# Kernel tuning notes

Hardware: AMD Instinct MI355X
Metric: run time of the kernel (lower is better)

## Reference

```python
import jax, jax.numpy as jnp
import numpy as np

NUM_EMBEDDINGS = 1024
EMBEDDING_DIM = 256
BETA = 0.25


def setup_inputs() -> dict:
    key = jax.random.key(0)
    k1, k2 = jax.random.split(key)
    inputs = jax.random.normal(k1, (32, EMBEDDING_DIM, 64, 64), dtype=jnp.float32)
    # codebook init: uniform(-1/K, 1/K), matching nn.Embedding init in the module
    embedding = jax.random.uniform(
        k2, (NUM_EMBEDDINGS, EMBEDDING_DIM), dtype=jnp.float32,
        minval=-1.0 / NUM_EMBEDDINGS, maxval=1.0 / NUM_EMBEDDINGS)
    return {"inputs": inputs, "embedding": embedding, "beta": BETA}


def reference(inputs, embedding, beta):
    # inputs: [B, D, H, W] -> [B, H, W, D]
    x = jnp.transpose(inputs, (0, 2, 3, 1))
    in_shape = x.shape
    flat = x.reshape(-1, embedding.shape[1])  # [N, D]
    dist = (jnp.sum(flat * flat, axis=1, keepdims=True)
            + jnp.sum(embedding * embedding, axis=1)
            - 2.0 * flat @ embedding.T)
    codebook_indices = jnp.argmin(dist, axis=1)  # [N]
    quantized = embedding[codebook_indices].reshape(in_shape)  # [B,H,W,D]
    sg = jax.lax.stop_gradient
    e_latent_loss = beta * jnp.mean((sg(quantized) - x) ** 2)
    q_latent_loss = jnp.mean((quantized - sg(x)) ** 2)
    loss = e_latent_loss + q_latent_loss
    # straight-through estimator
    quantized_st = x + sg(quantized - x)
    return loss, jnp.transpose(quantized_st, (0, 3, 1, 2))
```

## Files before the change

### kernel.cpp

```cpp
#include <hip/hip_runtime.h>


#define DIN 256

typedef __attribute__((ext_vector_type(8))) short short8;
typedef __attribute__((ext_vector_type(4))) float float4v;
typedef __attribute__((ext_vector_type(4))) unsigned short ushort4v;

static __device__ __forceinline__ unsigned short f2bf(float f) {
  unsigned int u = __float_as_uint(f);
  unsigned int r = (u + 0x7fffu + ((u >> 16) & 1u)) >> 16;
  return (unsigned short)r;
}

__global__ void vq_prep(const float* __restrict__ e,
                        unsigned short* __restrict__ e_pre,
                        float* __restrict__ norms) {
  int wave = threadIdx.x >> 6, lane = threadIdx.x & 63;
  int k = blockIdx.x * 4 + wave;
  const float4v* src = (const float4v*)(e + k * DIN);
  float4v v = src[lane];
  float ss = v[0]*v[0] + v[1]*v[1] + v[2]*v[2] + v[3]*v[3];
  ushort4v pk;
  pk[0] = f2bf(v[0]); pk[1] = f2bf(v[1]); pk[2] = f2bf(v[2]); pk[3] = f2bf(v[3]);
  int t = k >> 5, kL = k & 31;
  int cc = lane >> 1, half = lane & 1;
  int s = cc ^ (kL & 7);
  *(ushort4v*)(e_pre + t * 8192 + kL * 256 + s * 8 + half * 4) = pk;
  #pragma unroll
  for (int m = 1; m < 64; m <<= 1) ss += __shfl_xor(ss, m, 64);
  if (lane == 0) norms[k] = ss;
}

#define BARRIER_RAW() do { asm volatile("" ::: "memory"); \
  __builtin_amdgcn_s_barrier(); asm volatile("" ::: "memory"); } while (0)

__global__ void __launch_bounds__(512, 4)
vq_main(const float* __restrict__ xin, const float* __restrict__ e_fp,
        const unsigned short* __restrict__ e_pre,
        const float* __restrict__ norms,
        float* __restrict__ out, float* __restrict__ loss_acc) {
  __shared__ char smem[41024];
  unsigned short* xs = (unsigned short*)smem;
  float* qs  = (float*)smem;
  float* nrm = (float*)(smem + 32768);
  float* xnp = (float*)(smem + 36864);
  int*   fi  = (int*)(smem + 38912);
  float* xna = (float*)(smem + 39936);
  float* prt = (float*)(smem + 40960);

  const int tid  = threadIdx.x;
  const int wave = tid >> 6, lane = tid & 63;
  const int m16  = lane & 15, quad = lane >> 4;
  const int line0 = blockIdx.x * 4;

  nrm[tid] = norms[tid];
  nrm[tid + 512] = norms[tid + 512];

  short8 areg[16];
  const int wL  = wave >> 1;
  const int w32 = (wave & 1) * 32;
  {
    const int w  = tid & 63;
    const int cg = wave;
    for (int L = 0; L < 4; ++L) {
      int line = line0 + L;
      const float* xl = xin + (line >> 6) * 1048576 + (line & 63) * 64;
      __syncthreads();
      float ss = 0.0f;
      #pragma unroll
      for (int q8 = 0; q8 < 4; ++q8) {
        int cc = cg * 4 + q8;
        short8 pk;
        #pragma unroll
        for (int ii = 0; ii < 8; ++ii) {
          float xv = xl[(cc * 8 + ii) * 4096 + w];
          ss += xv * xv;
          pk[ii] = (short)f2bf(xv);
        }
        *(short8*)(xs + w * 256 + 8 * (cc ^ (w & 7))) = pk;
      }
      xnp[w * 8 + cg] = ss;
      __syncthreads();
      if (wL == L) {
        #pragma unroll
        for (int i = 0; i < 2; ++i)
          #pragma unroll
          for (int kk = 0; kk < 8; ++kk) {
            int r = w32 + i * 16 + m16;
            areg[i * 8 + kk] =
                *(short8*)(xs + r * 256 + 8 * ((kk * 4 + quad) ^ (r & 7)));
          }
      }
      if (tid < 64) {
        float s2 = 0.0f;
        #pragma unroll
        for (int u = 0; u < 8; ++u) s2 += xnp[tid * 8 + u];
        xna[L * 64 + tid] = s2;
      }
    }
  }
  __syncthreads();

  float bestv[2][4];
  int   besti[2][4];
  #pragma unroll
  for (int i = 0; i < 2; ++i)
    #pragma unroll
    for (int r = 0; r < 4; ++r) { bestv[i][r] = INFINITY; besti[i][r] = 0; }

  auto stage = [&](int t, int buf) {
    const char* src = (const char*)e_pre + t * 16384;
    char* dst = smem + buf * 16384;
    #pragma unroll
    for (int j = 0; j < 2; ++j) {
      int off = (j * 8 + wave) * 1024 + lane * 16;
      __builtin_amdgcn_global_load_lds(
          (const __attribute__((address_space(1))) unsigned int*)(src + off),
          (__attribute__((address_space(3))) unsigned int*)(dst + off),
          16, 0, 0);
    }
  };

  stage(0, 0);
  for (int t = 0; t < 32; ++t) {
    if (t < 31) {
      stage(t + 1, (t + 1) & 1);
      asm volatile("s_waitcnt vmcnt(2)" ::: "memory");
    } else {
      asm volatile("s_waitcnt vmcnt(0)" ::: "memory");
    }
    BARRIER_RAW();
    const unsigned short* eb = (const unsigned short*)(smem + (t & 1) * 16384);
    #pragma unroll
    for (int j = 0; j < 2; ++j) {
      int cL = j * 16 + m16;
      float4v a0 = (float4v)(0.0f), a1 = (float4v)(0.0f);
      #pragma unroll
      for (int kk = 0; kk < 8; ++kk) {
        short8 bfr = *(const short8*)(eb + cL * 256 + 8 * ((kk * 4 + quad) ^ (cL & 7)));
        a0 = __builtin_amdgcn_mfma_f32_16x16x32_bf16(areg[kk],     bfr, a0, 0, 0, 0);
        a1 = __builtin_amdgcn_mfma_f32_16x16x32_bf16(areg[8 + kk], bfr, a1, 0, 0, 0);
      }
      int col = t * 32 + cL;
      float nj = nrm[col];
      #pragma unroll
      for (int r = 0; r < 4; ++r) {
        float s0 = nj - 2.0f * a0[r];
        if (s0 < bestv[0][r]) { bestv[0][r] = s0; besti[0][r] = col; }
        float s1 = nj - 2.0f * a1[r];
        if (s1 < bestv[1][r]) { bestv[1][r] = s1; besti[1][r] = col; }
      }
    }
    BARRIER_RAW();
  }

  #pragma unroll
  for (int msk = 1; msk <= 8; msk <<= 1) {
    #pragma unroll
    for (int i = 0; i < 2; ++i)
      #pragma unroll
      for (int r = 0; r < 4; ++r) {
        float ov = __shfl_xor(bestv[i][r], msk, 64);
        int   oi = __shfl_xor(besti[i][r], msk, 64);
        if (ov < bestv[i][r] || (ov == bestv[i][r] && oi < besti[i][r])) {
          bestv[i][r] = ov; besti[i][r] = oi;
        }
      }
  }

  float lsum = 0.0f;
  if (m16 == 0) {
    #pragma unroll
    for (int i = 0; i < 2; ++i)
      #pragma unroll
      for (int r = 0; r < 4; ++r) {
        int row = wave * 32 + i * 16 + quad * 4 + r;
        fi[row] = besti[i][r];
        lsum += bestv[i][r] + xna[row];
      }
  }
  #pragma unroll
  for (int msk = 1; msk < 64; msk <<= 1) lsum += __shfl_xor(lsum, msk, 64);
  if (lane == 0) prt[wave] = lsum;
  __syncthreads();
  if (tid == 0) {
    float s = 0.0f;
    #pragma unroll
    for (int u = 0; u < 8; ++u) s += prt[u];
    atomicAdd(loss_acc, s);
  }

  for (int L = 0; L < 4; ++L) {
    int line = line0 + L;
    float* ob = out + 1 + (line >> 6) * 1048576 + (line & 63) * 64;
    int w = tid >> 3, dg = tid & 7;
    int idx = fi[L * 64 + w];
    const float* er = e_fp + idx * 256;
    int swz = (w >> 2) & 7;
    for (int h2 = 0; h2 < 2; ++h2) {
      #pragma unroll
      for (int j = 0; j < 4; ++j) {
        int c = dg + 8 * j;
        float4v qv = *(const float4v*)(er + h2 * 128 + c * 4);
        *(float4v*)(qs + w * 128 + (c ^ swz) * 4) = qv;
      }
      __syncthreads();
      #pragma unroll
      for (int it = 0; it < 4; ++it) {
        int dl = it * 32 + wave * 4 + quad;
        int slot = (dl >> 2) ^ (m16 & 7);
        float4v ov;
        #pragma unroll
        for (int k = 0; k < 4; ++k)
          ov[k] = qs[(m16 * 4 + k) * 128 + slot * 4 + (dl & 3)];
        *(float4v*)(ob + (h2 * 128 + dl) * 4096 + m16 * 4) = ov;
      }
      __syncthreads();
    }
  }
}

__global__ void vq_fin(const float* __restrict__ loss_acc,
                       const float* __restrict__ beta,
                       float* __restrict__ out) {
  out[0] = (1.0f + beta[0]) * loss_acc[0] / 33554432.0f;
}

extern "C" void kernel_launch(void* const* d_in, const int* in_sizes, int n_in,
                              void* d_out, int out_size, void* d_ws, size_t ws_size,
                              hipStream_t stream) {
  const float* xin  = (const float*)d_in[0];
  const float* emb  = (const float*)d_in[1];
  const float* beta = (const float*)d_in[2];
  float* out = (float*)d_out;
  float* loss_acc = (float*)d_ws;
  float* norms = (float*)((char*)d_ws + 4096);
  unsigned short* e_pre = (unsigned short*)((char*)d_ws + 8192);

  hipMemsetAsync(d_ws, 0, 4, stream);
  vq_prep<<<256, 256, 0, stream>>>(emb, e_pre, norms);
  vq_main<<<512, 512, 0, stream>>>(xin, emb, e_pre, norms, out, loss_acc);
  vq_fin<<<1, 1, 0, stream>>>(loss_acc, beta, out);
}
```

Measured before the change: 359.8 us.

## Halve block to 4 waves, each owning 64 rows loaded directly into registers

Moves the block from 8 waves to 4. Each wave now handles one full image line of 64 rows with four MFMA accumulator sets per codebook fragment, so every LDS-loaded codebook fragment feeds twice as many MFMAs. The input tile is read straight from global memory into A-fragment registers rather than staged through swizzled LDS, and the codebook prefetch now starts before that load. The output transpose is rewritten as a column-major LDS write followed by contiguous float4 stores. Costs are much higher register pressure (32 short8 A fragments plus 16 accumulators), 64KB of LDS per block, and lower occupancy.

```diff
diff --git a/kernel.cpp b/kernel.cpp
--- a/kernel.cpp
+++ b/kernel.cpp
@@ -35,98 +35,83 @@
 #define BARRIER_RAW() do { asm volatile("" ::: "memory"); \
   __builtin_amdgcn_s_barrier(); asm volatile("" ::: "memory"); } while (0)
 
-__global__ void __launch_bounds__(512, 4)
+__global__ void __launch_bounds__(256, 2)
 vq_main(const float* __restrict__ xin, const float* __restrict__ e_fp,
         const unsigned short* __restrict__ e_pre,
         const float* __restrict__ norms,
         float* __restrict__ out, float* __restrict__ loss_acc) {
-  __shared__ char smem[41024];
-  unsigned short* xs = (unsigned short*)smem;
+  __shared__ char smem[65536];
   float* qs  = (float*)smem;
   float* nrm = (float*)(smem + 32768);
-  float* xnp = (float*)(smem + 36864);
-  int*   fi  = (int*)(smem + 38912);
-  float* xna = (float*)(smem + 39936);
-  float* prt = (float*)(smem + 40960);
+  float* xna = (float*)(smem + 36864);
+  int*   fi  = (int*)(smem + 37888);
+  float* prt = (float*)(smem + 38912);
 
   const int tid  = threadIdx.x;
   const int wave = tid >> 6, lane = tid & 63;
   const int m16  = lane & 15, quad = lane >> 4;
   const int line0 = blockIdx.x * 4;
-
-  nrm[tid] = norms[tid];
-  nrm[tid + 512] = norms[tid + 512];
-
-  short8 areg[16];
-  const int wL  = wave >> 1;
-  const int w32 = (wave & 1) * 32;
-  {
-    const int w  = tid & 63;
-    const int cg = wave;
-    for (int L = 0; L < 4; ++L) {
-      int line = line0 + L;
-      const float* xl = xin + (line >> 6) * 1048576 + (line & 63) * 64;
-      __syncthreads();
-      float ss = 0.0f;
-      #pragma unroll
-      for (int q8 = 0; q8 < 4; ++q8) {
-        int cc = cg * 4 + q8;
-        short8 pk;
-        #pragma unroll
-        for (int ii = 0; ii < 8; ++ii) {
-          float xv = xl[(cc * 8 + ii) * 4096 + w];
-          ss += xv * xv;
-          pk[ii] = (short)f2bf(xv);
-        }
-        *(short8*)(xs + w * 256 + 8 * (cc ^ (w & 7))) = pk;
-      }
-      xnp[w * 8 + cg] = ss;
-      __syncthreads();
-      if (wL == L) {
-        #pragma unroll
-        for (int i = 0; i < 2; ++i)
-          #pragma unroll
-          for (int kk = 0; kk < 8; ++kk) {
-            int r = w32 + i * 16 + m16;
-            areg[i * 8 + kk] =
-                *(short8*)(xs + r * 256 + 8 * ((kk * 4 + quad) ^ (r & 7)));
-          }
-      }
-      if (tid < 64) {
-        float s2 = 0.0f;
-        #pragma unroll
-        for (int u = 0; u < 8; ++u) s2 += xnp[tid * 8 + u];
-        xna[L * 64 + tid] = s2;
-      }
-    }
-  }
-  __syncthreads();
-
-  float bestv[2][4];
-  int   besti[2][4];
-  #pragma unroll
-  for (int i = 0; i < 2; ++i)
-    #pragma unroll
-    for (int r = 0; r < 4; ++r) { bestv[i][r] = INFINITY; besti[i][r] = 0; }
+  const int line  = line0 + wave;
+  const float* xl = xin + (line >> 6) * 1048576 + (line & 63) * 64;
 
   auto stage = [&](int t, int buf) {
     const char* src = (const char*)e_pre + t * 16384;
     char* dst = smem + buf * 16384;
     #pragma unroll
-    for (int j = 0; j < 2; ++j) {
-      int off = (j * 8 + wave) * 1024 + lane * 16;
+    for (int j = 0; j < 4; ++j) {
+      int off = j * 4096 + tid * 16;
       __builtin_amdgcn_global_load_lds(
           (const __attribute__((address_space(1))) unsigned int*)(src + off),
           (__attribute__((address_space(3))) unsigned int*)(dst + off),
           16, 0, 0);
     }
   };
-
   stage(0, 0);
+
+  nrm[tid]       = norms[tid];
+  nrm[tid + 256] = norms[tid + 256];
+  nrm[tid + 512] = norms[tid + 512];
+  nrm[tid + 768] = norms[tid + 768];
+
+  short8 areg[32];
+  {
+    float ssq[4] = {0.0f, 0.0f, 0.0f, 0.0f};
+    #pragma unroll
+    for (int i = 0; i < 4; ++i) {
+      const float* p = xl + i * 16 + m16;
+      #pragma unroll
+      for (int kk = 0; kk < 8; ++kk) {
+        int dbase = kk * 32 + quad * 8;
+        short8 pk;
+        #pragma unroll
+        for (int ii = 0; ii < 8; ++ii) {
+          float xv = p[(dbase + ii) * 4096];
+          ssq[i] += xv * xv;
+          pk[ii] = (short)f2bf(xv);
+        }
+        areg[i * 8 + kk] = pk;
+      }
+    }
+    #pragma unroll
+    for (int i = 0; i < 4; ++i) {
+      float s = ssq[i];
+      s += __shfl_xor(s, 16, 64);
+      s += __shfl_xor(s, 32, 64);
+      if (quad == 0) xna[wave * 64 + i * 16 + m16] = s;
+    }
+  }
+
+  float bestv[4][4];
+  int   besti[4][4];
+  #pragma unroll
+  for (int i = 0; i < 4; ++i)
+    #pragma unroll
+    for (int r = 0; r < 4; ++r) { bestv[i][r] = INFINITY; besti[i][r] = 0; }
+
   for (int t = 0; t < 32; ++t) {
     if (t < 31) {
       stage(t + 1, (t + 1) & 1);
-      asm volatile("s_waitcnt vmcnt(2)" ::: "memory");
+      asm volatile("s_waitcnt vmcnt(4)" ::: "memory");
     } else {
       asm volatile("s_waitcnt vmcnt(0)" ::: "memory");
     }
@@ -136,11 +121,14 @@
     for (int j = 0; j < 2; ++j) {
       int cL = j * 16 + m16;
       float4v a0 = (float4v)(0.0f), a1 = (float4v)(0.0f);
+      float4v a2 = (float4v)(0.0f), a3 = (float4v)(0.0f);
       #pragma unroll
       for (int kk = 0; kk < 8; ++kk) {
         short8 bfr = *(const short8*)(eb + cL * 256 + 8 * ((kk * 4 + quad) ^ (cL & 7)));
-        a0 = __builtin_amdgcn_mfma_f32_16x16x32_bf16(areg[kk],     bfr, a0, 0, 0, 0);
-        a1 = __builtin_amdgcn_mfma_f32_16x16x32_bf16(areg[8 + kk], bfr, a1, 0, 0, 0);
+        a0 = __builtin_amdgcn_mfma_f32_16x16x32_bf16(areg[kk],      bfr, a0, 0, 0, 0);
+        a1 = __builtin_amdgcn_mfma_f32_16x16x32_bf16(areg[8 + kk],  bfr, a1, 0, 0, 0);
+        a2 = __builtin_amdgcn_mfma_f32_16x16x32_bf16(areg[16 + kk], bfr, a2, 0, 0, 0);
+        a3 = __builtin_amdgcn_mfma_f32_16x16x32_bf16(areg[24 + kk], bfr, a3, 0, 0, 0);
       }
       int col = t * 32 + cL;
       float nj = nrm[col];
@@ -150,6 +138,10 @@
         if (s0 < bestv[0][r]) { bestv[0][r] = s0; besti[0][r] = col; }
         float s1 = nj - 2.0f * a1[r];
         if (s1 < bestv[1][r]) { bestv[1][r] = s1; besti[1][r] = col; }
+        float s2 = nj - 2.0f * a2[r];
+        if (s2 < bestv[2][r]) { bestv[2][r] = s2; besti[2][r] = col; }
+        float s3 = nj - 2.0f * a3[r];
+        if (s3 < bestv[3][r]) { bestv[3][r] = s3; besti[3][r] = col; }
       }
     }
     BARRIER_RAW();
@@ -158,7 +150,7 @@
   #pragma unroll
   for (int msk = 1; msk <= 8; msk <<= 1) {
     #pragma unroll
-    for (int i = 0; i < 2; ++i)
+    for (int i = 0; i < 4; ++i)
       #pragma unroll
       for (int r = 0; r < 4; ++r) {
         float ov = __shfl_xor(bestv[i][r], msk, 64);
@@ -172,10 +164,10 @@
   float lsum = 0.0f;
   if (m16 == 0) {
     #pragma unroll
-    for (int i = 0; i < 2; ++i)
+    for (int i = 0; i < 4; ++i)
       #pragma unroll
       for (int r = 0; r < 4; ++r) {
-        int row = wave * 32 + i * 16 + quad * 4 + r;
+        int row = wave * 64 + i * 16 + quad * 4 + r;
         fi[row] = besti[i][r];
         lsum += bestv[i][r] + xna[row];
       }
@@ -184,39 +176,30 @@
   for (int msk = 1; msk < 64; msk <<= 1) lsum += __shfl_xor(lsum, msk, 64);
   if (lane == 0) prt[wave] = lsum;
   __syncthreads();
-  if (tid == 0) {
-    float s = 0.0f;
-    #pragma unroll
-    for (int u = 0; u < 8; ++u) s += prt[u];
-    atomicAdd(loss_acc, s);
-  }
-
-  for (int L = 0; L < 4; ++L) {
-    int line = line0 + L;
-    float* ob = out + 1 + (line >> 6) * 1048576 + (line & 63) * 64;
-    int w = tid >> 3, dg = tid & 7;
-    int idx = fi[L * 64 + w];
-    const float* er = e_fp + idx * 256;
-    int swz = (w >> 2) & 7;
-    for (int h2 = 0; h2 < 2; ++h2) {
-      #pragma unroll
-      for (int j = 0; j < 4; ++j) {
-        int c = dg + 8 * j;
-        float4v qv = *(const float4v*)(er + h2 * 128 + c * 4);
-        *(float4v*)(qs + w * 128 + (c ^ swz) * 4) = qv;
-      }
-      __syncthreads();
-      #pragma unroll
-      for (int it = 0; it < 4; ++it) {
-        int dl = it * 32 + wave * 4 + quad;
-        int slot = (dl >> 2) ^ (m16 & 7);
-        float4v ov;
-        #pragma unroll
-        for (int k = 0; k < 4; ++k)
-          ov[k] = qs[(m16 * 4 + k) * 128 + slot * 4 + (dl & 3)];
-        *(float4v*)(ob + (h2 * 128 + dl) * 4096 + m16 * 4) = ov;
-      }
-      __syncthreads();
+  if (tid == 0)
+    atomicAdd(loss_acc, prt[0] + prt[1] + prt[2] + prt[3]);
+
+  const int b0 = line0 >> 6, h0 = line0 & 63;
+  float* out1 = out + 1 + b0 * 1048576 + h0 * 64;
+  const int myidx = fi[tid];
+  const float* er = e_fp + myidx * 256;
+  __syncthreads();
+  for (int q = 0; q < 4; ++q) {
+    if (q) __syncthreads();
+    #pragma unroll
+    for (int c = 0; c < 16; ++c) {
+      float4v qv = *(const float4v*)(er + q * 64 + c * 4);
+      qs[(c * 4 + 0) * 256 + tid] = qv[0];
+      qs[(c * 4 + 1) * 256 + tid] = qv[1];
+      qs[(c * 4 + 2) * 256 + tid] = qv[2];
+      qs[(c * 4 + 3) * 256 + tid] = qv[3];
+    }
+    __syncthreads();
+    #pragma unroll
+    for (int it = 0; it < 16; ++it) {
+      int dl = it * 4 + wave;
+      float4v ov = *(const float4v*)(qs + dl * 256 + lane * 4);
+      *(float4v*)(out1 + (q * 64 + dl) * 4096 + lane * 4) = ov;
     }
   }
 }
@@ -240,6 +223,6 @@
 
   hipMemsetAsync(d_ws, 0, 4, stream);
   vq_prep<<<256, 256, 0, stream>>>(emb, e_pre, norms);
-  vq_main<<<512, 512, 0, stream>>>(xin, emb, e_pre, norms, out, loss_acc);
+  vq_main<<<512, 256, 0, stream>>>(xin, emb, e_pre, norms, out, loss_acc);
   vq_fin<<<1, 1, 0, stream>>>(loss_acc, beta, out);
 }
```

After: 360.7 us. No clear change (+0.2%).
